# Performance work log

Measured on AMD Instinct MI355X. Metric: run time of the kernel, lower is better.

## Reference

```python
import jax, jax.numpy as jnp
import numpy as np

EMBED_DIM = 1024
NUM_HEADS = 16
SEQ_LEN = 2048
BATCH = 2
LN_EPS = 1e-5


def setup_inputs() -> dict:
    key = jax.random.key(0)
    ks = jax.random.split(key, 12)
    d = EMBED_DIM
    s = 1.0 / np.sqrt(d)
    inp = {
        "x": jax.random.normal(ks[0], (BATCH, SEQ_LEN, d), dtype=jnp.float32),
        "ln1_g": jnp.ones((d,), jnp.float32),
        "ln1_b": jnp.zeros((d,), jnp.float32),
        "ln2_g": jnp.ones((d,), jnp.float32),
        "ln2_b": jnp.zeros((d,), jnp.float32),
        "W_qkv": jax.random.normal(ks[1], (d, 3 * d), jnp.float32) * s,
        "b_qkv": jnp.zeros((3 * d,), jnp.float32),
        "W_proj": jax.random.normal(ks[2], (d, d), jnp.float32) * s,
        "b_proj": jnp.zeros((d,), jnp.float32),
        "W_fc": jax.random.normal(ks[3], (d, 4 * d), jnp.float32) * s,
        "b_fc": jnp.zeros((4 * d,), jnp.float32),
        "W_out": jax.random.normal(ks[4], (4 * d, d), jnpp_dummy := jnp.float32) * (1.0 / np.sqrt(4 * d)),
        "b_out": jnp.zeros((d,), jnp.float32),
    }
    return inp


def _layernorm(x, g, b):
    mu = jnp.mean(x, axis=-1, keepdims=True)
    var = jnp.mean(jnp.square(x - mu), axis=-1, keepdims=True)
    return (x - mu) * jax.lax.rsqrt(var + LN_EPS) * g + b


def _block(x, ln1_g, ln1_b, ln2_g, ln2_b, W_qkv, b_qkv, W_proj, b_proj, W_fc, b_fc, W_out, b_out):
    B, S, D = x.shape
    H = NUM_HEADS
    hd = D // H
    h = _layernorm(x, ln1_g, ln1_b)
    qkv = h @ W_qkv + b_qkv  # [B,S,3D]
    q, k, v = jnp.split(qkv, 3, axis=-1)
    # [B,H,S,hd]
    q = q.reshape(B, S, H, hd).transpose(0, 2, 1, 3)
    k = k.reshape(B, S, H, hd).transpose(0, 2, 1, 3)
    v = v.reshape(B, S, H, hd).transpose(0, 2, 1, 3)
    attn = jnp.einsum("bhqd,bhkd->bhqk", q, k) / np.sqrt(hd).astype(np.float32)
    causal = jnp.tril(jnp.ones((S, S), dtype=bool))
    attn = jnp.where(causal, attn, -jnp.inf)
    attn = jax.nn.softmax(attn, axis=-1)
    y = jnp.einsum("bhqk,bhkd->bhqd", attn, v)
    y = y.transpose(0, 2, 1, 3).reshape(B, S, D)
    y = y @ W_proj + b_proj
    x = x + y
    h2 = _layernorm(x, ln2_g, ln2_b)
    m = jax.nn.relu(h2 @ W_fc + b_fc) @ W_out + b_out
    return x + m


def reference(x, ln1_g, ln1_b, ln2_g, ln2_b, W_qkv, b_qkv, W_proj, b_proj, W_fc, b_fc, W_out, b_out):
    return _block(x, ln1_g, ln1_b, ln2_g, ln2_b, W_qkv, b_qkv, W_proj, b_proj, W_fc, b_fc, W_out, b_out)
```

## Files before the change

kernel.cpp:

```cpp
#include <hip/hip_runtime.h>

typedef unsigned short u16;
typedef __attribute__((ext_vector_type(8))) __bf16 bf16x8;
typedef __attribute__((ext_vector_type(4))) float f32x4;

#define DEV __device__ __forceinline__

DEV u16 f2bf(float f) {
  unsigned u = __float_as_uint(f);
  u += 0x7fffu + ((u >> 16) & 1u);
  return (u16)(u >> 16);
}

DEV void gl_lds16(const void* g, void* l) {
  __builtin_amdgcn_global_load_lds(
      (const __attribute__((address_space(1))) void*)(uintptr_t)g,
      (__attribute__((address_space(3))) void*)(unsigned)(uintptr_t)l, 16, 0, 0);
}

DEV float wave_sum64(float v) {
#pragma unroll
  for (int off = 32; off > 0; off >>= 1) v += __shfl_down(v, off);
  return v;
}

__global__ __launch_bounds__(256) void ln_kernel(const float* __restrict__ x,
                                                 const float* __restrict__ g,
                                                 const float* __restrict__ be,
                                                 u16* __restrict__ out) {
  const int row = blockIdx.x, t = threadIdx.x;
  const int w = t >> 6, L = t & 63;
  __shared__ float red[8];
  const float4 v = reinterpret_cast<const float4*>(x + (size_t)row * 1024)[t];
  float s = v.x + v.y + v.z + v.w;
  s = wave_sum64(s);
  if (L == 0) red[w] = s;
  __syncthreads();
  const float mean = (red[0] + red[1] + red[2] + red[3]) * (1.0f / 1024.0f);
  const float dx = v.x - mean, dy = v.y - mean, dz = v.z - mean, dw = v.w - mean;
  float q = dx * dx + dy * dy + dz * dz + dw * dw;
  q = wave_sum64(q);
  if (L == 0) red[4 + w] = q;
  __syncthreads();
  const float var = (red[4] + red[5] + red[6] + red[7]) * (1.0f / 1024.0f);
  const float rs = rsqrtf(var + 1e-5f);
  const float4 gg = reinterpret_cast<const float4*>(g)[t];
  const float4 bb = reinterpret_cast<const float4*>(be)[t];
  ushort4 o;
  o.x = f2bf(dx * rs * gg.x + bb.x);
  o.y = f2bf(dy * rs * gg.y + bb.y);
  o.z = f2bf(dz * rs * gg.z + bb.z);
  o.w = f2bf(dw * rs * gg.w + bb.w);
  reinterpret_cast<ushort4*>(out + (size_t)row * 1024)[t] = o;
}

__global__ __launch_bounds__(256) void transpose_cvt(const float* __restrict__ W,
                                                     u16* __restrict__ Wt, int K, int N) {
  __shared__ float tile[32][33];
  const int c0 = blockIdx.x * 32, r0 = blockIdx.y * 32;
  const int tx = threadIdx.x & 31, ty = threadIdx.x >> 5;
#pragma unroll
  for (int j = 0; j < 4; ++j)
    tile[ty + j * 8][tx] = W[(size_t)(r0 + ty + j * 8) * N + c0 + tx];
  __syncthreads();
#pragma unroll
  for (int j = 0; j < 4; ++j) {
    const int n = c0 + ty + j * 8, k = r0 + tx;
    Wt[(size_t)n * K + k] = f2bf(tile[tx][ty + j * 8]);
  }
}

__global__ __launch_bounds__(256) void transpose_v(const u16* __restrict__ qkv,
                                                   u16* __restrict__ Vt) {
  __shared__ __attribute__((aligned(16))) u16 tile[64][72];
  const int s0 = blockIdx.x * 64;
  const int h = blockIdx.y, b = blockIdx.z;
  const int t = threadIdx.x;
#pragma unroll
  for (int i = 0; i < 2; ++i) {
    const int idx = i * 256 + t, r = idx >> 3, c = (idx & 7) << 3;
    const uint4 v =
        *(const uint4*)(qkv + (size_t)(b * 2048 + s0 + r) * 3072 + 2048 + h * 64 + c);
    *(uint4*)&tile[r][c] = v;
  }
  __syncthreads();
#pragma unroll
  for (int i = 0; i < 2; ++i) {
    const int idx = i * 256 + t, d = idx >> 3, sc = (idx & 7) << 3;
    u16 tmp[8];
#pragma unroll
    for (int j = 0; j < 8; ++j) tmp[j] = tile[sc + j][d];
    *(uint4*)(Vt + (size_t)((b * 16 + h) * 64 + d) * 2048 + s0 + sc) = *(uint4*)tmp;
  }
}

enum { F_BIAS = 1, F_RESID = 2, F_RELU = 4, F_BF16 = 8 };

template <int FLAGS>
__global__ __launch_bounds__(256, 2) void gemm_bt(const u16* __restrict__ A,
                                                  const u16* __restrict__ Bt,
                                                  const float* __restrict__ bias,
                                                  const float* __restrict__ resid,
                                                  void* __restrict__ Cout, int M, int N,
                                                  int K) {
  __shared__ __attribute__((aligned(16))) u16 sA[128 * 32];
  __shared__ __attribute__((aligned(16))) u16 sB[128 * 32];
  const int t = threadIdx.x, w = t >> 6, L = t & 63, quad = L >> 4, l15 = L & 15;
  const int wm = w >> 1, wn = w & 1;
  const int m0 = blockIdx.y * 128, n0 = blockIdx.x * 128;
  const u16* Ag = A + (size_t)m0 * K;
  const u16* Bg = Bt + (size_t)n0 * K;

  f32x4 acc[4][4] = {};

  for (int k0 = 0; k0 < K; k0 += 32) {
    __syncthreads();
#pragma unroll
    for (int i = 0; i < 2; ++i) {
      const int cp = i * 256 + t, rr = cp >> 2, cc = (cp & 3) << 3;
      gl_lds16(Ag + (size_t)rr * K + k0 + cc, &sA[(i * 256 + w * 64) * 8]);
    }
#pragma unroll
    for (int i = 0; i < 2; ++i) {
      const int cp = i * 256 + t, rr = cp >> 2, cc = (cp & 3) << 3;
      gl_lds16(Bg + (size_t)rr * K + k0 + cc, &sB[(i * 256 + w * 64) * 8]);
    }
    __syncthreads();

    bf16x8 af[4], bfr[4];
#pragma unroll
    for (int m = 0; m < 4; ++m)
      af[m] = *(const bf16x8*)&sA[(wm * 64 + m * 16 + l15) * 32 + quad * 8];
#pragma unroll
    for (int n = 0; n < 4; ++n)
      bfr[n] = *(const bf16x8*)&sB[(wn * 64 + n * 16 + l15) * 32 + quad * 8];
#pragma unroll
    for (int m = 0; m < 4; ++m)
#pragma unroll
      for (int n = 0; n < 4; ++n)
        acc[m][n] = __builtin_amdgcn_mfma_f32_16x16x32_bf16(af[m], bfr[n], acc[m][n], 0, 0, 0);
  }

#pragma unroll
  for (int m = 0; m < 4; ++m) {
#pragma unroll
    for (int n = 0; n < 4; ++n) {
      const int col = n0 + wn * 64 + n * 16 + l15;
      const float bv = (FLAGS & F_BIAS) ? bias[col] : 0.0f;
#pragma unroll
      for (int rr = 0; rr < 4; ++rr) {
        const int row = m0 + wm * 64 + m * 16 + quad * 4 + rr;
        float v = acc[m][n][rr] + bv;
        if (FLAGS & F_RESID) v += resid[(size_t)row * N + col];
        if (FLAGS & F_RELU) v = fmaxf(v, 0.0f);
        if (FLAGS & F_BF16)
          ((u16*)Cout)[(size_t)row * N + col] = f2bf(v);
        else
          ((float*)Cout)[(size_t)row * N + col] = v;
      }
    }
  }
}

__global__ __launch_bounds__(256) void flash_attn(const u16* __restrict__ qkv,
                                                  const u16* __restrict__ Vt,
                                                  u16* __restrict__ y) {
  constexpr int S = 2048, D3 = 3072, D = 1024;
  constexpr float Csc = 0.125f * 1.44269504088896f;
  __shared__ __attribute__((aligned(16))) u16 sK[2 * 64 * 32];
  __shared__ __attribute__((aligned(16))) u16 sV[2 * 64 * 32];
  __shared__ __attribute__((aligned(16))) u16 sP[4][2 * 16 * 40];

  const int lin = blockIdx.x;
  const int half = lin >> 9, rem = lin & 511;
  const int qt = half ? (31 - (rem & 31)) : (rem & 31);
  const int bh = (rem >> 5) | (half << 4);
  const int b = bh >> 4, h = bh & 15;
  const int q0 = qt * 64;

  const int t = threadIdx.x, w = t >> 6, L = t & 63, quad = L >> 4, l15 = L & 15;
  const int qw = q0 + w * 16;

  const u16* qbase = qkv + (size_t)(b * S) * D3 + h * 64;
  const u16* Kbase = qbase + D;
  const u16* Vbase = Vt + (size_t)((b * 16 + h) * 64) * S;

  bf16x8 aQ[2];
#pragma unroll
  for (int kk = 0; kk < 2; ++kk)
    aQ[kk] = *(const bf16x8*)(qbase + (size_t)(qw + l15) * D3 + kk * 32 + quad * 8);

  bf16x8 ones;
#pragma unroll
  for (int i = 0; i < 8; ++i) ones[i] = (__bf16)1.0f;

  f32x4 acc[4] = {};
  f32x4 lacc = {};

  u16* sPw = sP[w];
  const int nkv = qt + 1;
  for (int it = 0; it < nkv; ++it) {
    const int kv0 = it * 64;
    __syncthreads();
#pragma unroll
    for (int i = 0; i < 2; ++i) {
      const int cp = i * 256 + t;
      const int kk = cp >> 8, r = (cp >> 2) & 63, col = (cp & 3) << 3;
      gl_lds16(Kbase + (size_t)(kv0 + r) * D3 + kk * 32 + col, &sK[(i * 256 + w * 64) * 8]);
    }
#pragma unroll
    for (int i = 0; i < 2; ++i) {
      const int cp = i * 256 + t;
      const int kk = cp >> 8, d = (cp >> 2) & 63, col = (cp & 3) << 3;
      gl_lds16(Vbase + (size_t)d * S + kv0 + kk * 32 + col, &sV[(i * 256 + w * 64) * 8]);
    }
    __syncthreads();

    f32x4 s[4] = {};
#pragma unroll
    for (int kk = 0; kk < 2; ++kk) {
#pragma unroll
      for (int n = 0; n < 4; ++n) {
        const bf16x8 bK = *(const bf16x8*)&sK[kk * 2048 + (n * 16 + l15) * 32 + quad * 8];
        s[n] = __builtin_amdgcn_mfma_f32_16x16x32_bf16(aQ[kk], bK, s[n], 0, 0, 0);
      }
    }

    if (kv0 + 63 > qw) {
#pragma unroll
      for (int n = 0; n < 4; ++n) {
        const int col = kv0 + n * 16 + l15;
#pragma unroll
        for (int r = 0; r < 4; ++r) {
          const int row = qw + quad * 4 + r;
          const float p = __builtin_amdgcn_exp2f(s[n][r] * Csc);
          s[n][r] = (col > row) ? 0.0f : p;
        }
      }
    } else {
#pragma unroll
      for (int n = 0; n < 4; ++n)
#pragma unroll
        for (int r = 0; r < 4; ++r) s[n][r] = __builtin_amdgcn_exp2f(s[n][r] * Csc);
    }

#pragma unroll
    for (int n = 0; n < 4; ++n)
#pragma unroll
      for (int r = 0; r < 4; ++r)
        sPw[(n >> 1) * 640 + (quad * 4 + r) * 40 + (n & 1) * 16 + l15] = f2bf(s[n][r]);

#pragma unroll
    for (int kk = 0; kk < 2; ++kk) {
      const bf16x8 aP = *(const bf16x8*)&sPw[kk * 640 + l15 * 40 + quad * 8];
      lacc = __builtin_amdgcn_mfma_f32_16x16x32_bf16(aP, ones, lacc, 0, 0, 0);
#pragma unroll
      for (int dn = 0; dn < 4; ++dn) {
        const bf16x8 bV = *(const bf16x8*)&sV[kk * 2048 + (dn * 16 + l15) * 32 + quad * 8];
        acc[dn] = __builtin_amdgcn_mfma_f32_16x16x32_bf16(aP, bV, acc[dn], 0, 0, 0);
      }
    }
  }

#pragma unroll
  for (int r = 0; r < 4; ++r) {
    const float inv = 1.0f / lacc[r];
    const int row = qw + quad * 4 + r;
    u16* yb = y + (size_t)(b * S + row) * D + h * 64 + l15;
#pragma unroll
    for (int dn = 0; dn < 4; ++dn) yb[dn * 16] = f2bf(acc[dn][r] * inv);
  }
}

extern "C" void kernel_launch(void* const* d_in, const int* in_sizes, int n_in,
                              void* d_out, int out_size, void* d_ws, size_t ws_size,
                              hipStream_t stream) {
  const float* x = (const float*)d_in[0];
  const float* ln1g = (const float*)d_in[1];
  const float* ln1b = (const float*)d_in[2];
  const float* ln2g = (const float*)d_in[3];
  const float* ln2b = (const float*)d_in[4];
  const float* Wqkv = (const float*)d_in[5];
  const float* bqkv = (const float*)d_in[6];
  const float* Wproj = (const float*)d_in[7];
  const float* bproj = (const float*)d_in[8];
  const float* Wfc = (const float*)d_in[9];
  const float* bfc = (const float*)d_in[10];
  const float* Wout = (const float*)d_in[11];
  const float* bout = (const float*)d_in[12];

  char* ws = (char*)d_ws;
  u16* wt_qkv = (u16*)(ws + 0);
  u16* wt_proj = (u16*)(ws + 6291456);
  u16* wt_fc = (u16*)(ws + 8388608);
  u16* wt_out = (u16*)(ws + 16777216);
  u16* hbuf = (u16*)(ws + 25165824);
  float* x2 = (float*)(ws + 33554432);
  u16* ybuf = (u16*)(ws + 50331648);
  u16* qkvb = (u16*)(ws + 58720256);
  u16* vtb = (u16*)(ws + 83886080);
  u16* m1 = (u16*)(ws + 58720256);

  transpose_cvt<<<dim3(96, 32), 256, 0, stream>>>(Wqkv, wt_qkv, 1024, 3072);
  transpose_cvt<<<dim3(32, 32), 256, 0, stream>>>(Wproj, wt_proj, 1024, 1024);
  transpose_cvt<<<dim3(128, 32), 256, 0, stream>>>(Wfc, wt_fc, 1024, 4096);
  transpose_cvt<<<dim3(32, 128), 256, 0, stream>>>(Wout, wt_out, 4096, 1024);

  ln_kernel<<<4096, 256, 0, stream>>>(x, ln1g, ln1b, hbuf);
  gemm_bt<F_BIAS | F_BF16>
      <<<dim3(24, 32), 256, 0, stream>>>(hbuf, wt_qkv, bqkv, nullptr, qkvb, 4096, 3072, 1024);
  transpose_v<<<dim3(32, 16, 2), 256, 0, stream>>>(qkvb, vtb);
  flash_attn<<<1024, 256, 0, stream>>>(qkvb, vtb, ybuf);
  gemm_bt<F_BIAS | F_RESID>
      <<<dim3(8, 32), 256, 0, stream>>>(ybuf, wt_proj, bproj, x, x2, 4096, 1024, 1024);
  ln_kernel<<<4096, 256, 0, stream>>>(x2, ln2g, ln2b, hbuf);
  gemm_bt<F_BIAS | F_RELU | F_BF16>
      <<<dim3(32, 32), 256, 0, stream>>>(hbuf, wt_fc, bfc, nullptr, m1, 4096, 4096, 1024);
  gemm_bt<F_BIAS | F_RESID>
      <<<dim3(8, 32), 256, 0, stream>>>(m1, wt_out, bout, x2, (float*)d_out, 4096, 1024, 4096);
}
```

Before: 370.9 us.

## Split-K the projection and MLP-out GEMMs with atomic accumulation

The two N=1024 GEMMs (attention projection and MLP output) launched only 256 blocks, which underfills the GPU. They now split K across blockIdx.z (2 and 4 splits) and accumulate partial sums with float atomics into an output that a new kernel pre-fills with residual plus bias. This trades more blocks for extra atomic traffic, an additional elementwise pass per GEMM, and a summation order that is no longer deterministic.

```diff
diff --git a/kernel.cpp b/kernel.cpp
--- a/kernel.cpp
+++ b/kernel.cpp
@@ -54,6 +54,17 @@
   reinterpret_cast<ushort4*>(out + (size_t)row * 1024)[t] = o;
 }
 
+__global__ __launch_bounds__(256) void addbias_kernel(const float* __restrict__ src,
+                                                      const float* __restrict__ bias,
+                                                      float* __restrict__ dst) {
+  const int row = blockIdx.x, t = threadIdx.x;
+  const float4 v = reinterpret_cast<const float4*>(src + (size_t)row * 1024)[t];
+  const float4 b = reinterpret_cast<const float4*>(bias)[t];
+  float4 o;
+  o.x = v.x + b.x; o.y = v.y + b.y; o.z = v.z + b.z; o.w = v.w + b.w;
+  reinterpret_cast<float4*>(dst + (size_t)row * 1024)[t] = o;
+}
+
 __global__ __launch_bounds__(256) void transpose_cvt(const float* __restrict__ W,
                                                      u16* __restrict__ Wt, int K, int N) {
   __shared__ float tile[32][33];
@@ -94,7 +105,7 @@
   }
 }
 
-enum { F_BIAS = 1, F_RESID = 2, F_RELU = 4, F_BF16 = 8 };
+enum { F_BIAS = 1, F_RESID = 2, F_RELU = 4, F_BF16 = 8, F_ATOMIC = 16 };
 
 template <int FLAGS>
 __global__ __launch_bounds__(256, 2) void gemm_bt(const u16* __restrict__ A,
@@ -102,14 +113,14 @@
                                                   const float* __restrict__ bias,
                                                   const float* __restrict__ resid,
                                                   void* __restrict__ Cout, int M, int N,
-                                                  int K) {
+                                                  int K, int Kst) {
   __shared__ __attribute__((aligned(16))) u16 sA[128 * 32];
   __shared__ __attribute__((aligned(16))) u16 sB[128 * 32];
   const int t = threadIdx.x, w = t >> 6, L = t & 63, quad = L >> 4, l15 = L & 15;
   const int wm = w >> 1, wn = w & 1;
   const int m0 = blockIdx.y * 128, n0 = blockIdx.x * 128;
-  const u16* Ag = A + (size_t)m0 * K;
-  const u16* Bg = Bt + (size_t)n0 * K;
+  const u16* Ag = A + (size_t)m0 * Kst + (size_t)blockIdx.z * K;
+  const u16* Bg = Bt + (size_t)n0 * Kst + (size_t)blockIdx.z * K;
 
   f32x4 acc[4][4] = {};
 
@@ -118,12 +129,12 @@
 #pragma unroll
     for (int i = 0; i < 2; ++i) {
       const int cp = i * 256 + t, rr = cp >> 2, cc = (cp & 3) << 3;
-      gl_lds16(Ag + (size_t)rr * K + k0 + cc, &sA[(i * 256 + w * 64) * 8]);
+      gl_lds16(Ag + (size_t)rr * Kst + k0 + cc, &sA[(i * 256 + w * 64) * 8]);
     }
 #pragma unroll
     for (int i = 0; i < 2; ++i) {
       const int cp = i * 256 + t, rr = cp >> 2, cc = (cp & 3) << 3;
-      gl_lds16(Bg + (size_t)rr * K + k0 + cc, &sB[(i * 256 + w * 64) * 8]);
+      gl_lds16(Bg + (size_t)rr * Kst + k0 + cc, &sB[(i * 256 + w * 64) * 8]);
     }
     __syncthreads();
 
@@ -150,13 +161,17 @@
 #pragma unroll
       for (int rr = 0; rr < 4; ++rr) {
         const int row = m0 + wm * 64 + m * 16 + quad * 4 + rr;
-        float v = acc[m][n][rr] + bv;
-        if (FLAGS & F_RESID) v += resid[(size_t)row * N + col];
-        if (FLAGS & F_RELU) v = fmaxf(v, 0.0f);
-        if (FLAGS & F_BF16)
-          ((u16*)Cout)[(size_t)row * N + col] = f2bf(v);
-        else
-          ((float*)Cout)[(size_t)row * N + col] = v;
+        if (FLAGS & F_ATOMIC) {
+          unsafeAtomicAdd(&((float*)Cout)[(size_t)row * N + col], acc[m][n][rr]);
+        } else {
+          float v = acc[m][n][rr] + bv;
+          if (FLAGS & F_RESID) v += resid[(size_t)row * N + col];
+          if (FLAGS & F_RELU) v = fmaxf(v, 0.0f);
+          if (FLAGS & F_BF16)
+            ((u16*)Cout)[(size_t)row * N + col] = f2bf(v);
+          else
+            ((float*)Cout)[(size_t)row * N + col] = v;
+        }
       }
     }
   }
@@ -308,14 +323,19 @@
 
   ln_kernel<<<4096, 256, 0, stream>>>(x, ln1g, ln1b, hbuf);
   gemm_bt<F_BIAS | F_BF16>
-      <<<dim3(24, 32), 256, 0, stream>>>(hbuf, wt_qkv, bqkv, nullptr, qkvb, 4096, 3072, 1024);
+      <<<dim3(24, 32), 256, 0, stream>>>(hbuf, wt_qkv, bqkv, nullptr, qkvb, 4096, 3072, 1024, 1024);
   transpose_v<<<dim3(32, 16, 2), 256, 0, stream>>>(qkvb, vtb);
   flash_attn<<<1024, 256, 0, stream>>>(qkvb, vtb, ybuf);
-  gemm_bt<F_BIAS | F_RESID>
-      <<<dim3(8, 32), 256, 0, stream>>>(ybuf, wt_proj, bproj, x, x2, 4096, 1024, 1024);
+
+  addbias_kernel<<<4096, 256, 0, stream>>>(x, bproj, x2);
+  gemm_bt<F_ATOMIC>
+      <<<dim3(8, 32, 2), 256, 0, stream>>>(ybuf, wt_proj, nullptr, nullptr, x2, 4096, 1024, 512, 1024);
+
   ln_kernel<<<4096, 256, 0, stream>>>(x2, ln2g, ln2b, hbuf);
   gemm_bt<F_BIAS | F_RELU | F_BF16>
-      <<<dim3(32, 32), 256, 0, stream>>>(hbuf, wt_fc, bfc, nullptr, m1, 4096, 4096, 1024);
-  gemm_bt<F_BIAS | F_RESID>
-      <<<dim3(8, 32), 256, 0, stream>>>(m1, wt_out, bout, x2, (float*)d_out, 4096, 1024, 4096);
-}
+      <<<dim3(32, 32), 256, 0, stream>>>(hbuf, wt_fc, bfc, nullptr, m1, 4096, 4096, 1024, 1024);
+
+  addbias_kernel<<<4096, 256, 0, stream>>>(x2, bout, (float*)d_out);
+  gemm_bt<F_ATOMIC>
+      <<<dim3(8, 32, 4), 256, 0, stream>>>(m1, wt_out, nullptr, nullptr, (float*)d_out, 4096, 1024, 1024, 4096);
+}
```

Result: slower. 403.4 us (+8.8%).
